# Optimization experiments

Hardware: AMD Instinct MI355X
Metric: run time of the kernel (lower is better)

## Reference

```python
import jax, jax.numpy as jnp
import numpy as np

NUM_GRAPHS = 2048
NODES_PER_GRAPH = 256
N_NODES = NUM_GRAPHS * NODES_PER_GRAPH
N_EDGES = 2 * N_NODES
F_IN = 768
HID = 128
N_CLS = 2


def setup_inputs() -> dict:
    key = jax.random.key(0)
    ks = jax.random.split(key, 12)
    x = jax.random.normal(ks[0], (N_NODES, F_IN), dtype=jnp.float32)
    edge_index = jax.random.randint(ks[1], (2, N_EDGES), 0, N_NODES, dtype=jnp.int32)
    batch = jnp.repeat(jnp.arange(NUM_GRAPHS, dtype=jnp.int32), NODES_PER_GRAPH)
    s = 1.0 / np.sqrt(F_IN)
    sh = 1.0 / np.sqrt(HID)
    s2h = 1.0 / np.sqrt(2 * HID)
    return {
        "x": x,
        "edge_index": edge_index,
        "batch": batch,
        # SAGEConv: lin_l (aggregated neighbors, with bias) + lin_r (root, no bias)
        "W_l": jax.random.uniform(ks[2], (F_IN, HID), jnp.float32, -s, s),
        "b_l": jax.random.uniform(ks[3], (HID,), jnp.float32, -s, s),
        "W_r": jax.random.uniform(ks[4], (F_IN, HID), jnp.float32, -s, s),
        "W0": jax.random.uniform(ks[5], (F_IN, HID), jnp.float32, -s, s),
        "b0": jax.random.uniform(ks[6], (HID,), jnp.float32, -s, s),
        "W1": jax.random.uniform(ks[7], (2 * HID, HID), jnp.float32, -s2h, s2h),
        "b1": jax.random.uniform(ks[8], (HID,), jnp.float32, -s2h, s2h),
        "W2": jax.random.uniform(ks[9], (HID, N_CLS), jnp.float32, -sh, sh),
        "b2": jax.random.uniform(ks[10], (HID,), jnp.float32, -sh, sh)[:N_CLS],
    }


def reference(x, edge_index, batch, W_l, b_l, W_r, W0, b0, W1, b1, W2, b2):
    n = x.shape[0]
    src, dst = edge_index[0], edge_index[1]
    # SAGEConv with mean aggregation: gather -> segment mean -> transform
    msg_sum = jax.ops.segment_sum(x[src], dst, num_segments=n)      # [N, F]
    cnt = jax.ops.segment_sum(jnp.ones((src.shape[0],), x.dtype), dst, num_segments=n)
    agg = msg_sum / jnp.maximum(cnt, 1.0)[:, None]
    h = jax.nn.relu(agg @ W_l + b_l + x @ W_r)                       # [N, H]
    # global max pool per graph
    pooled = jax.ops.segment_max(h, batch, num_segments=NUM_GRAPHS)  # [G, H]
    # root (news) node = first node of each graph (batch is sorted)
    roots = jnp.searchsorted(batch, jnp.arange(NUM_GRAPHS, dtype=batch.dtype))
    news = jax.nn.relu(x[roots] @ W0 + b0)                           # [G, H]
    z = jax.nn.relu(jnp.concatenate([pooled, news], axis=1) @ W1 + b1)
    return jax.nn.log_softmax(z @ W2 + b2, axis=-1)                  # [G, 2]
```

## Files before the change

kernel.cpp:

```cpp
#include <hip/hip_runtime.h>

#define NGRAPH 2048
#define NPG 256
#define NNODE (NGRAPH*NPG)
#define NEDGE (2*NNODE)
#define FIN 768
#define HID 128
#define SLOTS 64
#define BK 32
#define NKT (FIN/BK)

typedef __bf16 bf16x8 __attribute__((ext_vector_type(8)));
typedef __bf16 bf16x4 __attribute__((ext_vector_type(4)));
typedef float f32x4 __attribute__((ext_vector_type(4)));

__device__ __forceinline__ float bflo(unsigned v) {
    return __uint_as_float((v & 0xffffu) << 16);
}
__device__ __forceinline__ float bfhi(unsigned v) {
    return __uint_as_float(v & 0xffff0000u);
}

__global__ __launch_bounds__(256) void k_prep(
    const float* __restrict__ Wl, const float* __restrict__ Wr,
    const float* __restrict__ W0, __bf16* __restrict__ WbT,
    int* __restrict__ deg)
{
    int idx = blockIdx.x * 256 + threadIdx.x;
    deg[idx] = 0;
    if (idx < 384 * FIN) {
        int n = idx / FIN;
        int k = idx - n * FIN;
        float v;
        if (n < HID)            v = Wl[k * HID + n];
        else if (n < 2 * HID)   v = Wr[k * HID + (n - HID)];
        else                    v = W0[k * HID + (n - 2 * HID)];
        WbT[idx] = (__bf16)v;
    }
}

__global__ __launch_bounds__(512, 4) void k_gemm(
    const float* __restrict__ X, const __bf16* __restrict__ WbT,
    __bf16* __restrict__ Yl, __bf16* __restrict__ Yr,
    const int* __restrict__ ei, int* __restrict__ deg, int* __restrict__ elist)
{
    __shared__ __align__(16) char sm[49152];
    const int t = threadIdx.x;

    if (t < 256) {
        int e = blockIdx.x * 256 + t;
        int src = ei[e];
        int dst = ei[NEDGE + e];
        int pos = atomicAdd(deg + dst, 1);
        if (pos < SLOTS) elist[(size_t)pos * NNODE + dst] = src;
    }

    const int lane = t & 63;
    const int w = t >> 6;
    const int wr = w >> 2;
    const int wc = w & 3;
    const size_t node0 = (size_t)blockIdx.x * 128;

    f32x4 acc[4][4];
#pragma unroll
    for (int m = 0; m < 4; ++m)
#pragma unroll
        for (int n = 0; n < 4; ++n)
            acc[m][n] = (f32x4){0.f, 0.f, 0.f, 0.f};

    const int arow = t >> 2;
    const int ak = (t & 3) * 8;
    const float* asrc = X + (node0 + arow) * FIN + ak;
    const int aswz = ((arow >> 1) & 3) << 4;
    const int aoff = arow * 64 + ((ak * 2) ^ aswz);

#define STAGE_B(kt, buf)                                                     \
    {                                                                        \
        _Pragma("unroll")                                                    \
        for (int r = 0; r < 2; ++r) {                                        \
            int idx = r * 512 + t;                                           \
            int bn = idx >> 2, bj = idx & 3;                                 \
            int koff = (bj ^ ((bn >> 1) & 3)) << 3;                          \
            const __bf16* gp = WbT + bn * FIN + (kt) * BK + koff;            \
            __builtin_amdgcn_global_load_lds(                                \
                (__attribute__((address_space(1))) void*)gp,                 \
                (__attribute__((address_space(3))) void*)((buf) + 8192 + idx * 16),\
                16, 0, 0);                                                   \
        }                                                                    \
    }

    f32x4 q0, q1;
    STAGE_B(0, sm);
    {
        const f32x4* s4 = (const f32x4*)asrc;
        q0 = s4[0]; q1 = s4[1];
        bf16x8 h;
#pragma unroll
        for (int i = 0; i < 4; ++i) { h[i] = (__bf16)q0[i]; h[4 + i] = (__bf16)q1[i]; }
        *(bf16x8*)(sm + aoff) = h;
    }
    __syncthreads();

    int cur = 0;
    for (int kt = 0; kt < NKT; ++kt) {
        char* bufC = sm + cur * 24576;
        char* bufN = sm + (cur ^ 1) * 24576;
        const bool more = (kt + 1 < NKT);

        if (more) {
            STAGE_B(kt + 1, bufN);
            const f32x4* s4 = (const f32x4*)(asrc + (kt + 1) * BK);
            q0 = s4[0]; q1 = s4[1];
            __builtin_amdgcn_sched_barrier(0);
        }

        const int kb = (lane >> 4) << 4;
        bf16x8 a[4], b[4];
#pragma unroll
        for (int m = 0; m < 4; ++m) {
            int row = wr * 64 + m * 16 + (lane & 15);
            a[m] = *(const bf16x8*)(bufC + row * 64 + (kb ^ (((row >> 1) & 3) << 4)));
        }
#pragma unroll
        for (int n = 0; n < 4; ++n) {
            int col = wc * 64 + n * 16 + (lane & 15);
            b[n] = *(const bf16x8*)(bufC + 8192 + col * 64 + (kb ^ (((col >> 1) & 3) << 4)));
        }
#pragma unroll
        for (int m = 0; m < 4; ++m)
#pragma unroll
            for (int n = 0; n < 4; ++n)
                acc[m][n] = __builtin_amdgcn_mfma_f32_16x16x32_bf16(
                    a[m], b[n], acc[m][n], 0, 0, 0);

        if (more) {
            bf16x8 h;
#pragma unroll
            for (int i = 0; i < 4; ++i) { h[i] = (__bf16)q0[i]; h[4 + i] = (__bf16)q1[i]; }
            *(bf16x8*)(bufN + aoff) = h;
        }
        __syncthreads();
        cur ^= 1;
    }

#pragma unroll
    for (int m = 0; m < 4; ++m) {
        const int rbase = wr * 64 + m * 16 + ((lane >> 4) << 2);
#pragma unroll
        for (int n = 0; n < 4; ++n) {
            const int col = wc * 64 + n * 16 + (lane & 15);
            __bf16* dst = (col < HID) ? Yl : Yr;
            const int c = col & (HID - 1);
#pragma unroll
            for (int j = 0; j < 4; ++j)
                dst[(node0 + rbase + j) * HID + c] = (__bf16)acc[m][n][j];
        }
    }
#undef STAGE_B
}

__global__ __launch_bounds__(512) void k_news(
    const float* __restrict__ X, const __bf16* __restrict__ W0bT,
    const float* __restrict__ b0, float* __restrict__ news)
{
    __shared__ __align__(16) char sm[12288];
    const int t = threadIdx.x;
    const int lane = t & 63;
    const int w = t >> 6;
    const int wr = w >> 2;
    const int wc = w & 3;
    const int g0 = blockIdx.x * 64;

    f32x4 acc[2][2];
#pragma unroll
    for (int m = 0; m < 2; ++m)
#pragma unroll
        for (int n = 0; n < 2; ++n)
            acc[m][n] = (f32x4){0.f, 0.f, 0.f, 0.f};

    const int arow = t >> 3;
    const int ak = (t & 7) * 4;
    const float* asrc = X + (size_t)(g0 + arow) * (NPG * FIN) + ak;
    const int aoff = arow * 64 + (((ak * 2) ^ (((arow >> 1) & 3) << 4)));

    for (int kt = 0; kt < NKT; ++kt) {
        const int k0 = kt * BK;
        __syncthreads();
        {
            f32x4 p = *(const f32x4*)(asrc + k0);
            bf16x4 h;
#pragma unroll
            for (int i = 0; i < 4; ++i) h[i] = (__bf16)p[i];
            *(bf16x4*)(sm + aoff) = h;
        }
        {
            int bn = t >> 2;
            int bj = t & 3;
            int koff = (bj ^ ((bn >> 1) & 3)) << 3;
            const __bf16* g = W0bT + bn * FIN + k0 + koff;
            __builtin_amdgcn_global_load_lds(
                (__attribute__((address_space(1))) void*)g,
                (__attribute__((address_space(3))) void*)(sm + 4096 + t * 16),
                16, 0, 0);
        }
        __syncthreads();

        const int kb = (lane >> 4) << 4;
        bf16x8 a[2], b[2];
#pragma unroll
        for (int m = 0; m < 2; ++m) {
            int row = wr * 32 + m * 16 + (lane & 15);
            a[m] = *(const bf16x8*)(sm + row * 64 + (kb ^ (((row >> 1) & 3) << 4)));
        }
#pragma unroll
        for (int n = 0; n < 2; ++n) {
            int row = wc * 32 + n * 16 + (lane & 15);
            b[n] = *(const bf16x8*)(sm + 4096 + row * 64 + (kb ^ (((row >> 1) & 3) << 4)));
        }
#pragma unroll
        for (int m = 0; m < 2; ++m)
#pragma unroll
            for (int n = 0; n < 2; ++n)
                acc[m][n] = __builtin_amdgcn_mfma_f32_16x16x32_bf16(
                    a[m], b[n], acc[m][n], 0, 0, 0);
    }

#pragma unroll
    for (int m = 0; m < 2; ++m) {
        const int rbase = wr * 32 + m * 16 + ((lane >> 4) << 2);
#pragma unroll
        for (int n = 0; n < 2; ++n) {
            const int col = wc * 32 + n * 16 + (lane & 15);
            const float bb = b0[col];
#pragma unroll
            for (int j = 0; j < 4; ++j)
                news[(size_t)(g0 + rbase + j) * HID + col] =
                    fmaxf(acc[m][n][j] + bb, 0.f);
        }
    }
}

__global__ __launch_bounds__(512) void k_fused(
    const int* __restrict__ deg, const int* __restrict__ elist,
    const __bf16* __restrict__ Yl, const __bf16* __restrict__ Yr,
    const float* __restrict__ bl, const float* __restrict__ news,
    const float* __restrict__ W1, const float* __restrict__ b1,
    const float* __restrict__ W2, const float* __restrict__ b2,
    float* __restrict__ out)
{
    __shared__ int   sdeg[NPG];
    __shared__ int   sel[4 * NPG];
    __shared__ float red[8 * HID];
    __shared__ float cat[2 * HID];
    __shared__ float zs[HID];

    const int g = blockIdx.x;
    const int t = threadIdx.x;
    const size_t gbase = (size_t)g * NPG;

    if (t < NPG) sdeg[t] = deg[gbase + t];
#pragma unroll
    for (int r = 0; r < 2; ++r) {
        int idx = r * 512 + t;
        sel[idx] = elist[(size_t)(idx >> 8) * NNODE + gbase + (idx & 255)];
    }
    __syncthreads();

    const int l = t & 63;
    const int sub = t >> 6;
    const int half = l >> 5;
    const int lj = l & 31;
    const int d4 = lj * 4;
    const float4 blv = *(const float4*)(bl + d4);
    const uint2* yl2 = (const uint2*)Yl;
    const uint2* yr2 = (const uint2*)Yr;

    float m0 = -3.0e38f, m1 = -3.0e38f, m2 = -3.0e38f, m3 = -3.0e38f;

    for (int k4 = 0; k4 < 8; ++k4) {
        const int nA = sub + 8 * (4 * k4 + half);
        const int nB = sub + 8 * (4 * k4 + 2 + half);
        const int dgA = sdeg[nA], dgB = sdeg[nB];
        int sA[4], sB[4];
#pragma unroll
        for (int j = 0; j < 4; ++j) {
            int cA = sel[j * NPG + nA];
            int cB = sel[j * NPG + nB];
            sA[j] = (j < dgA) ? cA : 0;
            sB[j] = (j < dgB) ? cB : 0;
        }
        uint2 vA[4], vB[4];
#pragma unroll
        for (int j = 0; j < 4; ++j) {
            vA[j] = yl2[(size_t)sA[j] * 32 + lj];
            vB[j] = yl2[(size_t)sB[j] * 32 + lj];
        }
        const uint2 yA = yr2[(gbase + nA) * 32 + lj];
        const uint2 yB = yr2[(gbase + nB) * 32 + lj];

        float s0A = 0.f, s1A = 0.f, s2A = 0.f, s3A = 0.f;
        float s0B = 0.f, s1B = 0.f, s2B = 0.f, s3B = 0.f;
#pragma unroll
        for (int j = 0; j < 4; ++j) {
            const float mA = (j < dgA) ? 1.f : 0.f;
            const float mB = (j < dgB) ? 1.f : 0.f;
            s0A = fmaf(mA, bflo(vA[j].x), s0A);
            s1A = fmaf(mA, bfhi(vA[j].x), s1A);
            s2A = fmaf(mA, bflo(vA[j].y), s2A);
            s3A = fmaf(mA, bfhi(vA[j].y), s3A);
            s0B = fmaf(mB, bflo(vB[j].x), s0B);
            s1B = fmaf(mB, bfhi(vB[j].x), s1B);
            s2B = fmaf(mB, bflo(vB[j].y), s2B);
            s3B = fmaf(mB, bfhi(vB[j].y), s3B);
        }
        int mx = dgA > dgB ? dgA : dgB;
        mx = max(mx, __shfl_xor(mx, 32));
        mx = mx < SLOTS ? mx : SLOTS;
        for (int j = 4; j < mx; ++j) {
            int cA = elist[(size_t)j * NNODE + gbase + nA];
            int cB = elist[(size_t)j * NNODE + gbase + nB];
            int eA = (j < dgA) ? cA : 0;
            int eB = (j < dgB) ? cB : 0;
            uint2 wA = yl2[(size_t)eA * 32 + lj];
            uint2 wB = yl2[(size_t)eB * 32 + lj];
            const float mA = (j < dgA) ? 1.f : 0.f;
            const float mB = (j < dgB) ? 1.f : 0.f;
            s0A = fmaf(mA, bflo(wA.x), s0A);
            s1A = fmaf(mA, bfhi(wA.x), s1A);
            s2A = fmaf(mA, bflo(wA.y), s2A);
            s3A = fmaf(mA, bfhi(wA.y), s3A);
            s0B = fmaf(mB, bflo(wB.x), s0B);
            s1B = fmaf(mB, bfhi(wB.x), s1B);
            s2B = fmaf(mB, bflo(wB.y), s2B);
            s3B = fmaf(mB, bfhi(wB.y), s3B);
        }
        const float invA = 1.f / fmaxf((float)dgA, 1.f);
        const float invB = 1.f / fmaxf((float)dgB, 1.f);
        float h0 = fmaf(s0A, invA, blv.x) + bflo(yA.x);
        float h1 = fmaf(s1A, invA, blv.y) + bfhi(yA.x);
        float h2 = fmaf(s2A, invA, blv.z) + bflo(yA.y);
        float h3 = fmaf(s3A, invA, blv.w) + bfhi(yA.y);
        m0 = fmaxf(m0, fmaxf(h0, 0.f));
        m1 = fmaxf(m1, fmaxf(h1, 0.f));
        m2 = fmaxf(m2, fmaxf(h2, 0.f));
        m3 = fmaxf(m3, fmaxf(h3, 0.f));
        h0 = fmaf(s0B, invB, blv.x) + bflo(yB.x);
        h1 = fmaf(s1B, invB, blv.y) + bfhi(yB.x);
        h2 = fmaf(s2B, invB, blv.z) + bflo(yB.y);
        h3 = fmaf(s3B, invB, blv.w) + bfhi(yB.y);
        m0 = fmaxf(m0, fmaxf(h0, 0.f));
        m1 = fmaxf(m1, fmaxf(h1, 0.f));
        m2 = fmaxf(m2, fmaxf(h2, 0.f));
        m3 = fmaxf(m3, fmaxf(h3, 0.f));
    }
    m0 = fmaxf(m0, __shfl_xor(m0, 32));
    m1 = fmaxf(m1, __shfl_xor(m1, 32));
    m2 = fmaxf(m2, __shfl_xor(m2, 32));
    m3 = fmaxf(m3, __shfl_xor(m3, 32));
    if (half == 0) {
        float4 mv = {m0, m1, m2, m3};
        *(float4*)(red + sub * HID + d4) = mv;
    }
    __syncthreads();

    if (t < HID) {
        float v = red[t];
#pragma unroll
        for (int s = 1; s < 8; ++s) v = fmaxf(v, red[s * HID + t]);
        cat[t] = v;
        cat[HID + t] = news[(size_t)g * HID + t];
    }
    __syncthreads();

    if (t < HID) {
        float a0 = 0.f, a1 = 0.f, a2 = 0.f, a3 = 0.f;
        for (int k = 0; k < 2 * HID; k += 4) {
            a0 = fmaf(cat[k + 0], W1[(k + 0) * HID + t], a0);
            a1 = fmaf(cat[k + 1], W1[(k + 1) * HID + t], a1);
            a2 = fmaf(cat[k + 2], W1[(k + 2) * HID + t], a2);
            a3 = fmaf(cat[k + 3], W1[(k + 3) * HID + t], a3);
        }
        zs[t] = fmaxf((a0 + a1) + (a2 + a3) + b1[t], 0.f);
    }
    __syncthreads();

    if (t < 64) {
        float z0 = zs[t * 2], z1 = zs[t * 2 + 1];
        float p0 = fmaf(z0, W2[t * 4 + 0], z1 * W2[t * 4 + 2]);
        float p1 = fmaf(z0, W2[t * 4 + 1], z1 * W2[t * 4 + 3]);
#pragma unroll
        for (int off = 32; off; off >>= 1) {
            p0 += __shfl_down(p0, off);
            p1 += __shfl_down(p1, off);
        }
        if (t == 0) {
            float l0 = p0 + b2[0], l1 = p1 + b2[1];
            float mx = fmaxf(l0, l1);
            float lse = mx + logf(expf(l0 - mx) + expf(l1 - mx));
            out[(size_t)g * 2 + 0] = l0 - lse;
            out[(size_t)g * 2 + 1] = l1 - lse;
        }
    }
}

extern "C" void kernel_launch(void* const* d_in, const int* in_sizes, int n_in,
                              void* d_out, int out_size, void* d_ws, size_t ws_size,
                              hipStream_t stream)
{
    const float* x   = (const float*)d_in[0];
    const int*   ei  = (const int*)d_in[1];
    const float* W_l = (const float*)d_in[3];
    const float* b_l = (const float*)d_in[4];
    const float* W_r = (const float*)d_in[5];
    const float* W0  = (const float*)d_in[6];
    const float* b0  = (const float*)d_in[7];
    const float* W1  = (const float*)d_in[8];
    const float* b1  = (const float*)d_in[9];
    const float* W2  = (const float*)d_in[10];
    const float* b2  = (const float*)d_in[11];
    float* out = (float*)d_out;

    char* ws = (char*)d_ws;
    size_t off = 0;
    auto alloc = [&](size_t bytes) {
        char* p = ws + off;
        off += (bytes + 511) & ~(size_t)511;
        return p;
    };
    __bf16* WbT   = (__bf16*)alloc((size_t)384 * FIN * 2);
    __bf16* Yl    = (__bf16*)alloc((size_t)NNODE * HID * 2);
    __bf16* Yr    = (__bf16*)alloc((size_t)NNODE * HID * 2);
    int*    deg   = (int*)alloc((size_t)NNODE * 4);
    int*    elist = (int*)alloc((size_t)NNODE * SLOTS * 4);
    float*  news  = (float*)alloc((size_t)NGRAPH * HID * 4);
    if (off > ws_size) return;

    k_prep<<<NNODE / 256, 256, 0, stream>>>(W_l, W_r, W0, WbT, deg);
    k_gemm<<<NNODE / 128, 512, 0, stream>>>(x, WbT, Yl, Yr, ei, deg, elist);
    k_news<<<NGRAPH / 64, 512, 0, stream>>>(x, WbT + (size_t)256 * FIN, b0, news);
    k_fused<<<NGRAPH, 512, 0, stream>>>(deg, elist, Yl, Yr, b_l, news,
                                        W1, b1, W2, b2, out);
}
```

Before: 685.7 us.

## Enlarge GEMM tile to 256 rows and K-step 64 with dynamic LDS

The node-feature GEMM block now handles 256 nodes instead of 128, and the K tile grows from 32 to 64. Each wave computes an 8x4 grid of MFMA tiles with new swizzled LDS layouts, using 128 KB of dynamic shared memory for double buffering. The aim is more reuse of the weight tile, fewer sync iterations, and fewer blocks overall. In exchange, occupancy drops to one block per CU, the kernel uses far more registers and LDS, and global-load latency has fewer waves available to hide it.

Result: faster. 668.8 us (-2.5%).

```diff
diff --git a/kernel.cpp b/kernel.cpp
--- a/kernel.cpp
+++ b/kernel.cpp
@@ -7,7 +7,7 @@
 #define FIN 768
 #define HID 128
 #define SLOTS 64
-#define BK 32
+#define BK 64
 #define NKT (FIN/BK)
 
 typedef __bf16 bf16x8 __attribute__((ext_vector_type(8)));
@@ -39,16 +39,16 @@
     }
 }
 
-__global__ __launch_bounds__(512, 4) void k_gemm(
+__global__ __launch_bounds__(512, 1) void k_gemm(
     const float* __restrict__ X, const __bf16* __restrict__ WbT,
     __bf16* __restrict__ Yl, __bf16* __restrict__ Yr,
     const int* __restrict__ ei, int* __restrict__ deg, int* __restrict__ elist)
 {
-    __shared__ __align__(16) char sm[49152];
+    extern __shared__ __align__(16) char sm[];
     const int t = threadIdx.x;
 
-    if (t < 256) {
-        int e = blockIdx.x * 256 + t;
+    {
+        int e = blockIdx.x * 512 + t;
         int src = ei[e];
         int dst = ei[NEDGE + e];
         int pos = atomicAdd(deg + dst, 1);
@@ -59,93 +59,114 @@
     const int w = t >> 6;
     const int wr = w >> 2;
     const int wc = w & 3;
-    const size_t node0 = (size_t)blockIdx.x * 128;
-
-    f32x4 acc[4][4];
-#pragma unroll
-    for (int m = 0; m < 4; ++m)
+    const size_t node0 = (size_t)blockIdx.x * 256;
+
+    f32x4 acc[8][4];
+#pragma unroll
+    for (int m = 0; m < 8; ++m)
 #pragma unroll
         for (int n = 0; n < 4; ++n)
             acc[m][n] = (f32x4){0.f, 0.f, 0.f, 0.f};
 
-    const int arow = t >> 2;
-    const int ak = (t & 3) * 8;
-    const float* asrc = X + (node0 + arow) * FIN + ak;
-    const int aswz = ((arow >> 1) & 3) << 4;
-    const int aoff = arow * 64 + ((ak * 2) ^ aswz);
+    const int arow = t >> 1;
+    const int half = t & 1;
+    const float* asrc = X + (node0 + arow) * FIN + half * 32;
+    const int aswz = (arow & 7) << 4;
+    int awoff[4];
+#pragma unroll
+    for (int j2 = 0; j2 < 4; ++j2)
+        awoff[j2] = arow * 128 + (((half * 4 + j2) * 16) ^ aswz);
 
 #define STAGE_B(kt, buf)                                                     \
     {                                                                        \
         _Pragma("unroll")                                                    \
-        for (int r = 0; r < 2; ++r) {                                        \
+        for (int r = 0; r < 4; ++r) {                                        \
             int idx = r * 512 + t;                                           \
-            int bn = idx >> 2, bj = idx & 3;                                 \
-            int koff = (bj ^ ((bn >> 1) & 3)) << 3;                          \
+            int bn = idx >> 3, bj = idx & 7;                                 \
+            int koff = (bj ^ (bn & 7)) << 3;                                 \
             const __bf16* gp = WbT + bn * FIN + (kt) * BK + koff;            \
             __builtin_amdgcn_global_load_lds(                                \
                 (__attribute__((address_space(1))) void*)gp,                 \
-                (__attribute__((address_space(3))) void*)((buf) + 8192 + idx * 16),\
+                (__attribute__((address_space(3))) void*)((buf) + 32768 + idx * 16),\
                 16, 0, 0);                                                   \
         }                                                                    \
     }
 
-    f32x4 q0, q1;
+    f32x4 q[8];
     STAGE_B(0, sm);
     {
         const f32x4* s4 = (const f32x4*)asrc;
-        q0 = s4[0]; q1 = s4[1];
-        bf16x8 h;
-#pragma unroll
-        for (int i = 0; i < 4; ++i) { h[i] = (__bf16)q0[i]; h[4 + i] = (__bf16)q1[i]; }
-        *(bf16x8*)(sm + aoff) = h;
+#pragma unroll
+        for (int i = 0; i < 8; ++i) q[i] = s4[i];
+#pragma unroll
+        for (int j2 = 0; j2 < 4; ++j2) {
+            bf16x8 h;
+#pragma unroll
+            for (int i = 0; i < 4; ++i) {
+                h[i]     = (__bf16)q[2 * j2][i];
+                h[4 + i] = (__bf16)q[2 * j2 + 1][i];
+            }
+            *(bf16x8*)(sm + awoff[j2]) = h;
+        }
     }
     __syncthreads();
 
     int cur = 0;
     for (int kt = 0; kt < NKT; ++kt) {
-        char* bufC = sm + cur * 24576;
-        char* bufN = sm + (cur ^ 1) * 24576;
+        char* bufC = sm + cur * 65536;
+        char* bufN = sm + (cur ^ 1) * 65536;
         const bool more = (kt + 1 < NKT);
 
         if (more) {
             STAGE_B(kt + 1, bufN);
+            __builtin_amdgcn_sched_barrier(0);
             const f32x4* s4 = (const f32x4*)(asrc + (kt + 1) * BK);
-            q0 = s4[0]; q1 = s4[1];
+#pragma unroll
+            for (int i = 0; i < 8; ++i) q[i] = s4[i];
             __builtin_amdgcn_sched_barrier(0);
         }
 
-        const int kb = (lane >> 4) << 4;
-        bf16x8 a[4], b[4];
-#pragma unroll
-        for (int m = 0; m < 4; ++m) {
-            int row = wr * 64 + m * 16 + (lane & 15);
-            a[m] = *(const bf16x8*)(bufC + row * 64 + (kb ^ (((row >> 1) & 3) << 4)));
-        }
-#pragma unroll
-        for (int n = 0; n < 4; ++n) {
-            int col = wc * 64 + n * 16 + (lane & 15);
-            b[n] = *(const bf16x8*)(bufC + 8192 + col * 64 + (kb ^ (((col >> 1) & 3) << 4)));
-        }
-#pragma unroll
-        for (int m = 0; m < 4; ++m)
-#pragma unroll
-            for (int n = 0; n < 4; ++n)
-                acc[m][n] = __builtin_amdgcn_mfma_f32_16x16x32_bf16(
-                    a[m], b[n], acc[m][n], 0, 0, 0);
+#pragma unroll
+        for (int ks = 0; ks < 2; ++ks) {
+            const int kb = ks * 64 + ((lane >> 4) << 4);
+            bf16x8 a[8], b[4];
+#pragma unroll
+            for (int m = 0; m < 8; ++m) {
+                int row = wr * 128 + m * 16 + (lane & 15);
+                a[m] = *(const bf16x8*)(bufC + row * 128 + (kb ^ ((row & 7) << 4)));
+            }
+#pragma unroll
+            for (int n = 0; n < 4; ++n) {
+                int col = wc * 64 + n * 16 + (lane & 15);
+                b[n] = *(const bf16x8*)(bufC + 32768 + col * 128 + (kb ^ ((col & 7) << 4)));
+            }
+#pragma unroll
+            for (int m = 0; m < 8; ++m)
+#pragma unroll
+                for (int n = 0; n < 4; ++n)
+                    acc[m][n] = __builtin_amdgcn_mfma_f32_16x16x32_bf16(
+                        a[m], b[n], acc[m][n], 0, 0, 0);
+        }
 
         if (more) {
-            bf16x8 h;
-#pragma unroll
-            for (int i = 0; i < 4; ++i) { h[i] = (__bf16)q0[i]; h[4 + i] = (__bf16)q1[i]; }
-            *(bf16x8*)(bufN + aoff) = h;
+#pragma unroll
+            for (int j2 = 0; j2 < 4; ++j2) {
+                bf16x8 h;
+#pragma unroll
+                for (int i = 0; i < 4; ++i) {
+                    h[i]     = (__bf16)q[2 * j2][i];
+                    h[4 + i] = (__bf16)q[2 * j2 + 1][i];
+                }
+                *(bf16x8*)(bufN + awoff[j2]) = h;
+            }
         }
         __syncthreads();
         cur ^= 1;
     }
 
 #pragma unroll
-    for (int m = 0; m < 4; ++m) {
-        const int rbase = wr * 64 + m * 16 + ((lane >> 4) << 2);
+    for (int m = 0; m < 8; ++m) {
+        const int rbase = wr * 128 + m * 16 + ((lane >> 4) << 2);
 #pragma unroll
         for (int n = 0; n < 4; ++n) {
             const int col = wc * 64 + n * 16 + (lane & 15);
@@ -183,8 +204,8 @@
     const float* asrc = X + (size_t)(g0 + arow) * (NPG * FIN) + ak;
     const int aoff = arow * 64 + (((ak * 2) ^ (((arow >> 1) & 3) << 4)));
 
-    for (int kt = 0; kt < NKT; ++kt) {
-        const int k0 = kt * BK;
+    for (int kt = 0; kt < FIN / 32; ++kt) {
+        const int k0 = kt * 32;
         __syncthreads();
         {
             f32x4 p = *(const f32x4*)(asrc + k0);
@@ -436,7 +457,7 @@
     if (off > ws_size) return;
 
     k_prep<<<NNODE / 256, 256, 0, stream>>>(W_l, W_r, W0, WbT, deg);
-    k_gemm<<<NNODE / 128, 512, 0, stream>>>(x, WbT, Yl, Yr, ei, deg, elist);
+    k_gemm<<<NNODE / 256, 512, 131072, stream>>>(x, WbT, Yl, Yr, ei, deg, elist);
     k_news<<<NGRAPH / 64, 512, 0, stream>>>(x, WbT + (size_t)256 * FIN, b0, news);
     k_fused<<<NGRAPH, 512, 0, stream>>>(deg, elist, Yl, Yr, b_l, news,
                                         W1, b1, W2, b2, out);
```
